# Kernel tuning notes

Hardware: AMD Instinct MI355X
Metric: run time of the kernel (lower is better)

The kernel has to match this reference:

```python
import jax, jax.numpy as jnp
import numpy as np
import math

NUM_HEADS = 16
ATTN_WIDTH = 256


def setup_inputs() -> dict:
    key = jax.random.key(0)
    ks = jax.random.split(key, 5)
    B, S, C, H = 2, 2048, 1024, 1024
    scale = 0.02
    return {
        "x": jax.random.normal(ks[0], (B, S, C), dtype=jnp.float32),
        "Wq": jax.random.normal(ks[1], (C, H), dtype=jnp.float32) * scale,
        "Wk": jax.random.normal(ks[2], (C, H), dtype=jnp.float32) * scale,
        "Wv": jax.random.normal(ks[3], (C, H), dtype=jnp.float32) * scale,
        "Wo": jax.random.normal(ks[4], (H, C), dtype=jnp.float32) * scale,
    }


def reference(x, Wq, Wk, Wv, Wo):
    B, S, C = x.shape
    H = NUM_HEADS
    dh = Wq.shape[1] // H  # head dim; Q.size(-1) in torch code

    def split_heads(t):
        # [B, S, H*dh] -> [B, H, S, dh]
        return t.reshape(B, S, H, dh).transpose(0, 2, 1, 3)

    q = split_heads(x @ Wq)
    k = split_heads(x @ Wk)
    v = split_heads(x @ Wv)

    scores = jnp.einsum("bhqd,bhkd->bhqk", q, k) / math.sqrt(dh)
    # exp-shift (first 'softmax-like' step, unnormalized)
    scores = jnp.exp(scores - jnp.max(scores, axis=-1, keepdims=True))
    # banded mask: tril(attn_width//2 - 1).triu(-(attn_width//2))
    i = jnp.arange(S)[:, None]
    j = jnp.arange(S)[None, :]
    d = j - i
    half = ATTN_WIDTH // 2
    mask = (d <= half - 1) & (d >= -half)
    scores = jnp.where(mask, scores, 0.0)
    # second softmax over the masked exp-scores (zeros contribute exp(0)=1)
    weights = jax.nn.softmax(scores, axis=-1)

    out = jnp.einsum("bhqk,bhkd->bhqd", weights, v)  # [B, H, S, dh]
    out = out.transpose(0, 2, 1, 3).reshape(B, S, H * dh)
    return out @ Wo
```

## Files before the change

kernel.cpp:

```cpp
#include <hip/hip_runtime.h>
#include <math.h>

typedef __bf16 bf16_t;
typedef bf16_t bf16x8 __attribute__((ext_vector_type(8)));
typedef bf16_t bf16x4 __attribute__((ext_vector_type(4)));
typedef float f32x4 __attribute__((ext_vector_type(4)));

constexpr int S_ = 2048;
constexpr float SCALE = 0.125f;

#define MFMA_B16(a, b, c) __builtin_amdgcn_mfma_f32_16x16x32_bf16(a, b, c, 0, 0, 0)

typedef __attribute__((address_space(1))) const void* as1_cvp;
typedef __attribute__((address_space(3))) void* as3_vp;

__device__ __forceinline__ void gl2lds16(const void* g, void* l)
{
    __builtin_amdgcn_global_load_lds((as1_cvp)g, (as3_vp)l, 16, 0, 0);
}

__global__ __launch_bounds__(256) void prep(const float* __restrict__ x,
                                            const float* __restrict__ Wq,
                                            const float* __restrict__ Wk,
                                            const float* __restrict__ Wv,
                                            const float* __restrict__ Wo,
                                            bf16_t* __restrict__ xb,
                                            bf16_t* __restrict__ Wqt,
                                            bf16_t* __restrict__ Wkt,
                                            bf16_t* __restrict__ Wvt,
                                            bf16_t* __restrict__ Wot,
                                            float* __restrict__ vsp)
{
    __shared__ float T[64][65];
    const int blk = blockIdx.x;
    const int tid = threadIdx.x;
    if (blk < 1024) {
#pragma unroll
        for (int u = 0; u < 4; ++u) {
            const int g = blk * 1024 + u * 256 + tid;
            const float4 v = ((const float4*)x)[g];
            bf16x4 o;
            o[0] = (bf16_t)v.x; o[1] = (bf16_t)v.y;
            o[2] = (bf16_t)v.z; o[3] = (bf16_t)v.w;
            *(bf16x4*)&xb[(size_t)g * 4] = o;
        }
    } else if (blk < 2048) {
        const int rem = blk - 1024;
        const int wsel = rem >> 8, t = rem & 255;
        const float* src = (wsel == 0) ? Wq : (wsel == 1) ? Wk : (wsel == 2) ? Wv : Wo;
        bf16_t* dst = (wsel == 0) ? Wqt : (wsel == 1) ? Wkt : (wsel == 2) ? Wvt : Wot;
        const int k0 = (t >> 4) * 64, n0 = (t & 15) * 64;
        const int rr = tid >> 4, c4 = (tid & 15) * 4;
#pragma unroll
        for (int u = 0; u < 4; ++u) {
            const float4 v = *(const float4*)&src[(size_t)(k0 + u * 16 + rr) * 1024 + n0 + c4];
            T[u * 16 + rr][c4 + 0] = v.x; T[u * 16 + rr][c4 + 1] = v.y;
            T[u * 16 + rr][c4 + 2] = v.z; T[u * 16 + rr][c4 + 3] = v.w;
        }
        __syncthreads();
#pragma unroll
        for (int u = 0; u < 4; ++u) {
            bf16x4 o;
#pragma unroll
            for (int e = 0; e < 4; ++e) o[e] = (bf16_t)T[c4 + e][u * 16 + rr];
            *(bf16x4*)&dst[(size_t)(n0 + u * 16 + rr) * 1024 + k0 + c4] = o;
        }
    } else {
#pragma unroll
        for (int u = 0; u < 8; ++u) vsp[u * 256 + tid] = 0.f;
    }
}

template <int MODE>
__device__ __forceinline__ void mfma_gemm_body(const bf16_t* __restrict__ A,
                                               const bf16_t* __restrict__ Bt,
                                               void* __restrict__ dst,
                                               float* __restrict__ vsum_out,
                                               int m0, int n0)
{
    __shared__ bf16_t As[4096];
    __shared__ bf16_t Bs[4096];

    const int tid = threadIdx.x;
    const int lane = tid & 63, wid = tid >> 6;
    const int l15 = lane & 15, quad = lane >> 4;
    const int wm = (wid & 1) * 64, wn = (wid >> 1) * 64;

    const int srow = wid * 32 + (lane >> 2);
    const int scg8 = (lane & 3) * 8;
    const bf16_t* Ag0 = A  + (size_t)(m0 + srow) * 1024 + scg8;
    const bf16_t* Ag1 = A  + (size_t)(m0 + srow + 16) * 1024 + scg8;
    const bf16_t* Bg0 = Bt + (size_t)(n0 + srow) * 1024 + scg8;
    const bf16_t* Bg1 = Bt + (size_t)(n0 + srow + 16) * 1024 + scg8;
    bf16_t* Al0 = As + (wid * 2 + 0) * 512;
    bf16_t* Al1 = As + (wid * 2 + 1) * 512;
    bf16_t* Bl0 = Bs + (wid * 2 + 0) * 512;
    bf16_t* Bl1 = Bs + (wid * 2 + 1) * 512;

    f32x4 acc[4][4];
#pragma unroll
    for (int i = 0; i < 4; ++i)
#pragma unroll
        for (int j = 0; j < 4; ++j) acc[i][j] = (f32x4){0.f, 0.f, 0.f, 0.f};

    for (int k0 = 0; k0 < 1024; k0 += 32) {
        __syncthreads();
        gl2lds16(Ag0 + k0, Al0);
        gl2lds16(Ag1 + k0, Al1);
        gl2lds16(Bg0 + k0, Bl0);
        gl2lds16(Bg1 + k0, Bl1);
        __syncthreads();

        bf16x8 af[4], bfr[4];
#pragma unroll
        for (int mt = 0; mt < 4; ++mt)
            af[mt] = *(const bf16x8*)&As[(wm + mt * 16 + l15) * 32 + quad * 8];
#pragma unroll
        for (int nt = 0; nt < 4; ++nt)
            bfr[nt] = *(const bf16x8*)&Bs[(wn + nt * 16 + l15) * 32 + quad * 8];
#pragma unroll
        for (int mt = 0; mt < 4; ++mt)
#pragma unroll
            for (int nt = 0; nt < 4; ++nt)
                acc[mt][nt] = MFMA_B16(bfr[nt], af[mt], acc[mt][nt]);
    }

#pragma unroll
    for (int mt = 0; mt < 4; ++mt) {
        const int m = m0 + wm + mt * 16 + l15;
#pragma unroll
        for (int nt = 0; nt < 4; ++nt) {
            const int nb = n0 + wn + nt * 16 + quad * 4;
            if (MODE == 0) {
                *(f32x4*)&((float*)dst)[(size_t)m * 1024 + nb] = acc[mt][nt];
            } else {
                const int bb = m >> 11, s = m & 2047;
                const int hh = nb >> 6, d = nb & 63;
                bf16x4 o;
#pragma unroll
                for (int u = 0; u < 4; ++u) o[u] = (bf16_t)acc[mt][nt][u];
                *(bf16x4*)&((bf16_t*)dst)[((size_t)(bb * 16 + hh) * 2048 + s) * 64 + d] = o;
            }
        }
    }

    if (MODE == 1 && vsum_out != nullptr) {
        const int bb = m0 >> 11;
#pragma unroll
        for (int nt = 0; nt < 4; ++nt) {
            f32x4 p = acc[0][nt];
#pragma unroll
            for (int mt = 1; mt < 4; ++mt) {
                p[0] += acc[mt][nt][0]; p[1] += acc[mt][nt][1];
                p[2] += acc[mt][nt][2]; p[3] += acc[mt][nt][3];
            }
#pragma unroll
            for (int st = 1; st < 16; st <<= 1) {
                p[0] += __shfl_xor(p[0], st);
                p[1] += __shfl_xor(p[1], st);
                p[2] += __shfl_xor(p[2], st);
                p[3] += __shfl_xor(p[3], st);
            }
            if (l15 == 0) {
                const int nI = n0 + wn + nt * 16 + quad * 4;
                float* vp = &vsum_out[(bb * 16 + (nI >> 6)) * 64 + (nI & 63)];
                atomicAdd(vp + 0, p[0]);
                atomicAdd(vp + 1, p[1]);
                atomicAdd(vp + 2, p[2]);
                atomicAdd(vp + 3, p[3]);
            }
        }
    }
}

__global__ __launch_bounds__(256) void gemm_qkv_mfma(const bf16_t* __restrict__ xb,
                                                     const bf16_t* __restrict__ Wqt,
                                                     const bf16_t* __restrict__ Wkt,
                                                     const bf16_t* __restrict__ Wvt,
                                                     bf16_t* Qh, bf16_t* Kh, bf16_t* Vh,
                                                     float* vsp)
{
    const bf16_t* Bt = (blockIdx.z == 0) ? Wqt : (blockIdx.z == 1) ? Wkt : Wvt;
    bf16_t* dst = (blockIdx.z == 0) ? Qh : (blockIdx.z == 1) ? Kh : Vh;
    float* vs = (blockIdx.z == 2) ? vsp : nullptr;
    mfma_gemm_body<1>(xb, Bt, dst, vs, blockIdx.y * 128, blockIdx.x * 128);
}

__global__ __launch_bounds__(256) void gemm_out_mfma(const bf16_t* __restrict__ attn,
                                                     const bf16_t* __restrict__ Wot,
                                                     float* __restrict__ out)
{
    mfma_gemm_body<0>(attn, Wot, out, nullptr, blockIdx.y * 128, blockIdx.x * 128);
}

__global__ __launch_bounds__(256) void attn_fused(const bf16_t* __restrict__ Qh,
                                                  const bf16_t* __restrict__ Kh,
                                                  const bf16_t* __restrict__ Vh,
                                                  const float* __restrict__ vsp,
                                                  bf16_t* __restrict__ attn)
{
    __shared__ bf16_t Qs[4096];
    __shared__ bf16_t Kbig[16384];
    __shared__ float msh[4][4][16];
    __shared__ float zsh[4][16];

    bf16_t* Ks2 = Kbig;
    bf16_t* Vt  = Kbig + 4096;
    bf16_t* Wsm = Kbig + 8704;

    const int tid = threadIdx.x;
    const int lane = tid & 63, wid = tid >> 6;
    const int l15 = lane & 15, quad = lane >> 4;
    const int b = blockIdx.z, h = blockIdx.y, bh = b * 16 + h;
    const int i0 = blockIdx.x * 64;
    const bf16_t* Qb = Qh + (size_t)bh * 131072;
    const bf16_t* Kb = Kh + (size_t)bh * 131072;
    const bf16_t* Vb = Vh + (size_t)bh * 131072;

#pragma unroll
    for (int c = 0; c < 2; ++c) {
        const int g = (wid * 2 + c) * 64 + lane;
        const int half = g >> 8, rem = g & 255;
        const int row = rem >> 2, c8 = rem & 3;
        gl2lds16(Qb + (size_t)(i0 + row) * 64 + half * 32 + c8 * 8,
                 Qs + (wid * 2 + c) * 512);
    }
    __syncthreads();

    bf16x8 af[4][2];
#pragma unroll
    for (int mt = 0; mt < 4; ++mt)
#pragma unroll
        for (int ks = 0; ks < 2; ++ks)
            af[mt][ks] = *(const bf16x8*)&Qs[ks * 2048 + (mt * 16 + l15) * 32 + quad * 8];

    float rmax[4] = {-3.0e38f, -3.0e38f, -3.0e38f, -3.0e38f};

    for (int jc = 0; jc < 8; ++jc) {
        __syncthreads();
#pragma unroll
        for (int c = 0; c < 8; ++c) {
            const int g = (wid * 8 + c) * 64 + lane;
            const int half = g >> 10, rem = g & 1023;
            const int row = rem >> 2, c8 = rem & 3;
            gl2lds16(Kb + (size_t)(jc * 256 + row) * 64 + half * 32 + c8 * 8,
                     Kbig + (size_t)(wid * 8 + c) * 512);
        }
        __syncthreads();
#pragma unroll
        for (int ntl = 0; ntl < 4; ++ntl) {
            const int nt = wid * 4 + ntl;
            const bf16x8 b0 = *(const bf16x8*)&Kbig[(nt * 16 + l15) * 32 + quad * 8];
            const bf16x8 b1 = *(const bf16x8*)&Kbig[8192 + (nt * 16 + l15) * 32 + quad * 8];
#pragma unroll
            for (int mt = 0; mt < 4; ++mt) {
                f32x4 t = (f32x4){0.f, 0.f, 0.f, 0.f};
                t = MFMA_B16(b0, af[mt][0], t);
                t = MFMA_B16(b1, af[mt][1], t);
                rmax[mt] = fmaxf(rmax[mt], fmaxf(fmaxf(t[0], t[1]), fmaxf(t[2], t[3])));
            }
        }
    }
#pragma unroll
    for (int mt = 0; mt < 4; ++mt) {
        float v = rmax[mt];
        v = fmaxf(v, __shfl_xor(v, 16));
        v = fmaxf(v, __shfl_xor(v, 32));
        if (quad == 0) msh[wid][mt][l15] = v;
    }
    __syncthreads();

    float mreg[4];
#pragma unroll
    for (int r = 0; r < 4; ++r) {
        const int il = quad * 4 + r;
        mreg[r] = SCALE * fmaxf(fmaxf(msh[0][wid][il], msh[1][wid][il]),
                                fmaxf(msh[2][wid][il], msh[3][wid][il]));
    }

    const bf16x8 aq0 = *(const bf16x8*)&Qs[(wid * 16 + l15) * 32 + quad * 8];
    const bf16x8 aq1 = *(const bf16x8*)&Qs[2048 + (wid * 16 + l15) * 32 + quad * 8];

    f32x4 vsd4[4];
#pragma unroll
    for (int nt = 0; nt < 4; ++nt)
        vsd4[nt] = *(const f32x4*)&vsp[bh * 64 + nt * 16 + quad * 4];

    f32x4 accO[4];
#pragma unroll
    for (int nt = 0; nt < 4; ++nt) accO[nt] = (f32x4){0.f, 0.f, 0.f, 0.f};
    float zp[4] = {0.f, 0.f, 0.f, 0.f};

    for (int cb = 0; cb < 5; ++cb) {
        const int jb = i0 - 128 + cb * 64;
        if (jb < 0 || jb >= S_) continue;

        __syncthreads();
#pragma unroll
        for (int c = 0; c < 2; ++c) {
            const int g = (wid * 2 + c) * 64 + lane;
            const int half = g >> 8, rem = g & 255;
            const int row = rem >> 2, c8 = rem & 3;
            gl2lds16(Kb + (size_t)(jb + row) * 64 + half * 32 + c8 * 8,
                     Ks2 + (wid * 2 + c) * 512);
        }
        {
            const bf16x8 v0 = *(const bf16x8*)&Vb[(size_t)(jb + lane) * 64 + wid * 16];
            const bf16x8 v1 = *(const bf16x8*)&Vb[(size_t)(jb + lane) * 64 + wid * 16 + 8];
#pragma unroll
            for (int e = 0; e < 8; ++e) {
                Vt[(wid * 16 + e) * 72 + lane] = v0[e];
                Vt[(wid * 16 + 8 + e) * 72 + lane] = v1[e];
            }
        }
        __syncthreads();

        f32x4 sacc[4];
#pragma unroll
        for (int nt = 0; nt < 4; ++nt) {
            const bf16x8 k0 = *(const bf16x8*)&Ks2[(nt * 16 + l15) * 32 + quad * 8];
            const bf16x8 k1 = *(const bf16x8*)&Ks2[2048 + (nt * 16 + l15) * 32 + quad * 8];
            f32x4 t = (f32x4){0.f, 0.f, 0.f, 0.f};
            t = MFMA_B16(aq0, k0, t);
            t = MFMA_B16(aq1, k1, t);
            sacc[nt] = t;
        }

#pragma unroll
        for (int nt = 0; nt < 4; ++nt) {
#pragma unroll
            for (int r = 0; r < 4; ++r) {
                const int ig = i0 + wid * 16 + quad * 4 + r;
                const int jg = jb + nt * 16 + l15;
                const int dd = jg - ig;
                const bool ok = (dd >= -128) && (dd <= 127);
                const float t = __expf(sacc[nt][r] * SCALE - mreg[r]);
                const float wv = ok ? (__expf(t) - 1.0f) : 0.0f;
                const bf16_t wb = (bf16_t)wv;
                zp[r] += (float)wb;
                Wsm[(wid * 16 + quad * 4 + r) * 72 + nt * 16 + l15] = wb;
            }
        }
        __syncthreads();

#pragma unroll
        for (int ks = 0; ks < 2; ++ks) {
            const bf16x8 aw = *(const bf16x8*)&Wsm[(wid * 16 + l15) * 72 + ks * 32 + quad * 8];
#pragma unroll
            for (int nt = 0; nt < 4; ++nt) {
                const bf16x8 bv = *(const bf16x8*)&Vt[(nt * 16 + l15) * 72 + ks * 32 + quad * 8];
                accO[nt] = MFMA_B16(bv, aw, accO[nt]);
            }
        }
    }

#pragma unroll
    for (int r = 0; r < 4; ++r) {
        float z = zp[r];
        z += __shfl_xor(z, 1);
        z += __shfl_xor(z, 2);
        z += __shfl_xor(z, 4);
        z += __shfl_xor(z, 8);
        if (l15 == 0) zsh[wid][quad * 4 + r] = z + (float)S_;
    }
    __syncthreads();
    const float rz = 1.0f / zsh[wid][l15];

    const int irow = i0 + wid * 16 + l15;
#pragma unroll
    for (int nt = 0; nt < 4; ++nt) {
        bf16x4 o;
#pragma unroll
        for (int r = 0; r < 4; ++r)
            o[r] = (bf16_t)((accO[nt][r] + vsd4[nt][r]) * rz);
        *(bf16x4*)&attn[(size_t)(b * S_ + irow) * 1024 + h * 64 + nt * 16 + quad * 4] = o;
    }
}

extern "C" void kernel_launch(void* const* d_in, const int* in_sizes, int n_in,
                              void* d_out, int out_size, void* d_ws, size_t ws_size,
                              hipStream_t stream)
{
    const float* x  = (const float*)d_in[0];
    const float* Wq = (const float*)d_in[1];
    const float* Wk = (const float*)d_in[2];
    const float* Wv = (const float*)d_in[3];
    const float* Wo = (const float*)d_in[4];
    float* out = (float*)d_out;

    char* ws = (char*)d_ws;
    bf16_t* xb   = (bf16_t*)(ws + 0);
    bf16_t* Wqt  = (bf16_t*)(ws + 8388608);
    bf16_t* Wkt  = (bf16_t*)(ws + 10485760);
    bf16_t* Wvt  = (bf16_t*)(ws + 12582912);
    bf16_t* Wot  = (bf16_t*)(ws + 14680064);
    bf16_t* Qh   = (bf16_t*)(ws + 16777216);
    bf16_t* Kh   = (bf16_t*)(ws + 25165824);
    bf16_t* Vh   = (bf16_t*)(ws + 33554432);
    bf16_t* attn = (bf16_t*)(ws + 41943040);
    float*  vsp  = (float*)(ws + 50331648);

    prep<<<2049, 256, 0, stream>>>(x, Wq, Wk, Wv, Wo, xb, Wqt, Wkt, Wvt, Wot, vsp);
    gemm_qkv_mfma<<<dim3(8, 32, 3), 256, 0, stream>>>(xb, Wqt, Wkt, Wvt, Qh, Kh, Vh, vsp);
    attn_fused<<<dim3(32, 16, 2), 256, 0, stream>>>(Qh, Kh, Vh, vsp, attn);
    gemm_out_mfma<<<dim3(8, 32), 256, 0, stream>>>(attn, Wot, out);
}
```

Before: 193.3 us.

## Double attention query tile to 128 rows and remap blocks for locality

Each attention block now handles 128 query rows instead of 64, with each wave owning two 16-row tiles. This halves the number of blocks that stream the full K sequence for the row-max pass, and lets each loaded V tile be reused across two query tiles. The grid is flattened to 512 blocks with an index remap that places consecutive blocks on different heads of the same batch, likely aimed at L2 locality. The cost is higher register pressure (Q fragments for 8 tiles, doubled accumulators) and fewer blocks to fill the GPU, partly offset by launch_bounds(256,2).

```diff
diff --git a/kernel.cpp b/kernel.cpp
--- a/kernel.cpp
+++ b/kernel.cpp
@@ -193,67 +193,73 @@
     mfma_gemm_body<0>(attn, Wot, out, nullptr, blockIdx.y * 128, blockIdx.x * 128);
 }
 
-__global__ __launch_bounds__(256) void attn_fused(const bf16_t* __restrict__ Qh,
-                                                  const bf16_t* __restrict__ Kh,
-                                                  const bf16_t* __restrict__ Vh,
-                                                  const float* __restrict__ vsp,
-                                                  bf16_t* __restrict__ attn)
-{
-    __shared__ bf16_t Qs[4096];
-    __shared__ bf16_t Kbig[16384];
-    __shared__ float msh[4][4][16];
-    __shared__ float zsh[4][16];
-
-    bf16_t* Ks2 = Kbig;
-    bf16_t* Vt  = Kbig + 4096;
-    bf16_t* Wsm = Kbig + 8704;
+__global__ __launch_bounds__(256, 2) void attn_fused(const bf16_t* __restrict__ Qh,
+                                                     const bf16_t* __restrict__ Kh,
+                                                     const bf16_t* __restrict__ Vh,
+                                                     const float* __restrict__ vsp,
+                                                     bf16_t* __restrict__ attn)
+{
+    __shared__ bf16_t Qs[8192];
+    __shared__ bf16_t pool[17920];
+    __shared__ float msh[4][8][16];
+    __shared__ float zsh[4][32];
+
+    bf16_t* Ks2 = pool;
+    bf16_t* Vt  = pool + 4096;
+    bf16_t* Ws  = pool + 8704;
 
     const int tid = threadIdx.x;
     const int lane = tid & 63, wid = tid >> 6;
     const int l15 = lane & 15, quad = lane >> 4;
-    const int b = blockIdx.z, h = blockIdx.y, bh = b * 16 + h;
-    const int i0 = blockIdx.x * 64;
+
+    const int f = blockIdx.x;
+    const int seq = f >> 3;
+    const int bh = (f & 7) + 8 * (seq >> 4);
+    const int i0 = (seq & 15) * 128;
+    const int b = bh >> 4, h = bh & 15;
     const bf16_t* Qb = Qh + (size_t)bh * 131072;
     const bf16_t* Kb = Kh + (size_t)bh * 131072;
     const bf16_t* Vb = Vh + (size_t)bh * 131072;
 
 #pragma unroll
-    for (int c = 0; c < 2; ++c) {
-        const int g = (wid * 2 + c) * 64 + lane;
-        const int half = g >> 8, rem = g & 255;
-        const int row = rem >> 2, c8 = rem & 3;
-        gl2lds16(Qb + (size_t)(i0 + row) * 64 + half * 32 + c8 * 8,
-                 Qs + (wid * 2 + c) * 512);
+    for (int c = 0; c < 4; ++c) {
+        const int g = wid * 4 + c;
+        const int half = g >> 3;
+        const int row = (g & 7) * 16 + (lane >> 2);
+        gl2lds16(Qb + (size_t)(i0 + row) * 64 + half * 32 + (lane & 3) * 8,
+                 Qs + g * 512);
     }
     __syncthreads();
 
-    bf16x8 af[4][2];
-#pragma unroll
-    for (int mt = 0; mt < 4; ++mt)
+    bf16x8 af[8][2];
+#pragma unroll
+    for (int mt = 0; mt < 8; ++mt)
 #pragma unroll
         for (int ks = 0; ks < 2; ++ks)
-            af[mt][ks] = *(const bf16x8*)&Qs[ks * 2048 + (mt * 16 + l15) * 32 + quad * 8];
-
-    float rmax[4] = {-3.0e38f, -3.0e38f, -3.0e38f, -3.0e38f};
+            af[mt][ks] = *(const bf16x8*)&Qs[ks * 4096 + (mt * 16 + l15) * 32 + quad * 8];
+
+    float rmax[8];
+#pragma unroll
+    for (int mt = 0; mt < 8; ++mt) rmax[mt] = -3.0e38f;
 
     for (int jc = 0; jc < 8; ++jc) {
         __syncthreads();
 #pragma unroll
         for (int c = 0; c < 8; ++c) {
-            const int g = (wid * 8 + c) * 64 + lane;
-            const int half = g >> 10, rem = g & 1023;
-            const int row = rem >> 2, c8 = rem & 3;
-            gl2lds16(Kb + (size_t)(jc * 256 + row) * 64 + half * 32 + c8 * 8,
-                     Kbig + (size_t)(wid * 8 + c) * 512);
+            const int g = wid * 8 + c;
+            const int half = g >> 4;
+            const int row = (g & 15) * 16 + (lane >> 2);
+            gl2lds16(Kb + (size_t)(jc * 256 + row) * 64 + half * 32 + (lane & 3) * 8,
+                     pool + g * 512);
         }
         __syncthreads();
 #pragma unroll
         for (int ntl = 0; ntl < 4; ++ntl) {
-            const int nt = wid * 4 + ntl;
-            const bf16x8 b0 = *(const bf16x8*)&Kbig[(nt * 16 + l15) * 32 + quad * 8];
-            const bf16x8 b1 = *(const bf16x8*)&Kbig[8192 + (nt * 16 + l15) * 32 + quad * 8];
-#pragma unroll
-            for (int mt = 0; mt < 4; ++mt) {
+            const int jt = wid * 4 + ntl;
+            const bf16x8 b0 = *(const bf16x8*)&pool[(jt * 16 + l15) * 32 + quad * 8];
+            const bf16x8 b1 = *(const bf16x8*)&pool[8192 + (jt * 16 + l15) * 32 + quad * 8];
+#pragma unroll
+            for (int mt = 0; mt < 8; ++mt) {
                 f32x4 t = (f32x4){0.f, 0.f, 0.f, 0.f};
                 t = MFMA_B16(b0, af[mt][0], t);
                 t = MFMA_B16(b1, af[mt][1], t);
@@ -262,7 +268,7 @@
         }
     }
 #pragma unroll
-    for (int mt = 0; mt < 4; ++mt) {
+    for (int mt = 0; mt < 8; ++mt) {
         float v = rmax[mt];
         v = fmaxf(v, __shfl_xor(v, 16));
         v = fmaxf(v, __shfl_xor(v, 32));
@@ -270,39 +276,41 @@
     }
     __syncthreads();
 
-    float mreg[4];
-#pragma unroll
-    for (int r = 0; r < 4; ++r) {
-        const int il = quad * 4 + r;
-        mreg[r] = SCALE * fmaxf(fmaxf(msh[0][wid][il], msh[1][wid][il]),
-                                fmaxf(msh[2][wid][il], msh[3][wid][il]));
-    }
-
-    const bf16x8 aq0 = *(const bf16x8*)&Qs[(wid * 16 + l15) * 32 + quad * 8];
-    const bf16x8 aq1 = *(const bf16x8*)&Qs[2048 + (wid * 16 + l15) * 32 + quad * 8];
+    float mreg[2][4];
+#pragma unroll
+    for (int t = 0; t < 2; ++t)
+#pragma unroll
+        for (int r = 0; r < 4; ++r) {
+            const int mt = wid * 2 + t;
+            const int il = quad * 4 + r;
+            mreg[t][r] = SCALE * fmaxf(fmaxf(msh[0][mt][il], msh[1][mt][il]),
+                                       fmaxf(msh[2][mt][il], msh[3][mt][il]));
+        }
 
     f32x4 vsd4[4];
 #pragma unroll
-    for (int nt = 0; nt < 4; ++nt)
-        vsd4[nt] = *(const f32x4*)&vsp[bh * 64 + nt * 16 + quad * 4];
-
-    f32x4 accO[4];
-#pragma unroll
-    for (int nt = 0; nt < 4; ++nt) accO[nt] = (f32x4){0.f, 0.f, 0.f, 0.f};
-    float zp[4] = {0.f, 0.f, 0.f, 0.f};
-
-    for (int cb = 0; cb < 5; ++cb) {
+    for (int dt = 0; dt < 4; ++dt)
+        vsd4[dt] = *(const f32x4*)&vsp[bh * 64 + dt * 16 + quad * 4];
+
+    f32x4 accO[2][4];
+#pragma unroll
+    for (int t = 0; t < 2; ++t)
+#pragma unroll
+        for (int dt = 0; dt < 4; ++dt) accO[t][dt] = (f32x4){0.f, 0.f, 0.f, 0.f};
+    float zp[2][4] = {{0.f, 0.f, 0.f, 0.f}, {0.f, 0.f, 0.f, 0.f}};
+
+    for (int cb = 0; cb < 6; ++cb) {
         const int jb = i0 - 128 + cb * 64;
         if (jb < 0 || jb >= S_) continue;
 
         __syncthreads();
 #pragma unroll
         for (int c = 0; c < 2; ++c) {
-            const int g = (wid * 2 + c) * 64 + lane;
-            const int half = g >> 8, rem = g & 255;
-            const int row = rem >> 2, c8 = rem & 3;
-            gl2lds16(Kb + (size_t)(jb + row) * 64 + half * 32 + c8 * 8,
-                     Ks2 + (wid * 2 + c) * 512);
+            const int g = wid * 2 + c;
+            const int half = g >> 2;
+            const int row = (g & 3) * 16 + (lane >> 2);
+            gl2lds16(Kb + (size_t)(jb + row) * 64 + half * 32 + (lane & 3) * 8,
+                     Ks2 + g * 512);
         }
         {
             const bf16x8 v0 = *(const bf16x8*)&Vb[(size_t)(jb + lane) * 64 + wid * 16];
@@ -315,65 +323,74 @@
         }
         __syncthreads();
 
-        f32x4 sacc[4];
-#pragma unroll
-        for (int nt = 0; nt < 4; ++nt) {
-            const bf16x8 k0 = *(const bf16x8*)&Ks2[(nt * 16 + l15) * 32 + quad * 8];
-            const bf16x8 k1 = *(const bf16x8*)&Ks2[2048 + (nt * 16 + l15) * 32 + quad * 8];
-            f32x4 t = (f32x4){0.f, 0.f, 0.f, 0.f};
-            t = MFMA_B16(aq0, k0, t);
-            t = MFMA_B16(aq1, k1, t);
-            sacc[nt] = t;
-        }
-
-#pragma unroll
-        for (int nt = 0; nt < 4; ++nt) {
-#pragma unroll
-            for (int r = 0; r < 4; ++r) {
-                const int ig = i0 + wid * 16 + quad * 4 + r;
-                const int jg = jb + nt * 16 + l15;
-                const int dd = jg - ig;
-                const bool ok = (dd >= -128) && (dd <= 127);
-                const float t = __expf(sacc[nt][r] * SCALE - mreg[r]);
-                const float wv = ok ? (__expf(t) - 1.0f) : 0.0f;
-                const bf16_t wb = (bf16_t)wv;
-                zp[r] += (float)wb;
-                Wsm[(wid * 16 + quad * 4 + r) * 72 + nt * 16 + l15] = wb;
+#pragma unroll
+        for (int t = 0; t < 2; ++t) {
+            const int mt = wid * 2 + t;
+#pragma unroll
+            for (int jt4 = 0; jt4 < 4; ++jt4) {
+                const bf16x8 k0 = *(const bf16x8*)&Ks2[(jt4 * 16 + l15) * 32 + quad * 8];
+                const bf16x8 k1 = *(const bf16x8*)&Ks2[2048 + (jt4 * 16 + l15) * 32 + quad * 8];
+                f32x4 sc = (f32x4){0.f, 0.f, 0.f, 0.f};
+                sc = MFMA_B16(af[mt][0], k0, sc);
+                sc = MFMA_B16(af[mt][1], k1, sc);
+#pragma unroll
+                for (int r = 0; r < 4; ++r) {
+                    const int ig = i0 + mt * 16 + quad * 4 + r;
+                    const int jg = jb + jt4 * 16 + l15;
+                    const int dd = jg - ig;
+                    const bool ok = (dd >= -128) && (dd <= 127);
+                    const float e1 = __expf(sc[r] * SCALE - mreg[t][r]);
+                    const float wv = ok ? (__expf(e1) - 1.0f) : 0.0f;
+                    const bf16_t wb = (bf16_t)wv;
+                    zp[t][r] += (float)wb;
+                    Ws[(mt * 16 + quad * 4 + r) * 72 + jt4 * 16 + l15] = wb;
+                }
             }
         }
         __syncthreads();
 
 #pragma unroll
         for (int ks = 0; ks < 2; ++ks) {
-            const bf16x8 aw = *(const bf16x8*)&Wsm[(wid * 16 + l15) * 72 + ks * 32 + quad * 8];
-#pragma unroll
-            for (int nt = 0; nt < 4; ++nt) {
-                const bf16x8 bv = *(const bf16x8*)&Vt[(nt * 16 + l15) * 72 + ks * 32 + quad * 8];
-                accO[nt] = MFMA_B16(bv, aw, accO[nt]);
-            }
-        }
-    }
-
-#pragma unroll
-    for (int r = 0; r < 4; ++r) {
-        float z = zp[r];
-        z += __shfl_xor(z, 1);
-        z += __shfl_xor(z, 2);
-        z += __shfl_xor(z, 4);
-        z += __shfl_xor(z, 8);
-        if (l15 == 0) zsh[wid][quad * 4 + r] = z + (float)S_;
-    }
+            bf16x8 bv[4];
+#pragma unroll
+            for (int dt = 0; dt < 4; ++dt)
+                bv[dt] = *(const bf16x8*)&Vt[(dt * 16 + l15) * 72 + ks * 32 + quad * 8];
+#pragma unroll
+            for (int t = 0; t < 2; ++t) {
+                const int mt = wid * 2 + t;
+                const bf16x8 aw = *(const bf16x8*)&Ws[(mt * 16 + l15) * 72 + ks * 32 + quad * 8];
+#pragma unroll
+                for (int dt = 0; dt < 4; ++dt)
+                    accO[t][dt] = MFMA_B16(bv[dt], aw, accO[t][dt]);
+            }
+        }
+    }
+
+#pragma unroll
+    for (int t = 0; t < 2; ++t)
+#pragma unroll
+        for (int r = 0; r < 4; ++r) {
+            float z = zp[t][r];
+            z += __shfl_xor(z, 1);
+            z += __shfl_xor(z, 2);
+            z += __shfl_xor(z, 4);
+            z += __shfl_xor(z, 8);
+            if (l15 == 0) zsh[wid][t * 16 + quad * 4 + r] = z + (float)S_;
+        }
     __syncthreads();
-    const float rz = 1.0f / zsh[wid][l15];
-
-    const int irow = i0 + wid * 16 + l15;
-#pragma unroll
-    for (int nt = 0; nt < 4; ++nt) {
-        bf16x4 o;
-#pragma unroll
-        for (int r = 0; r < 4; ++r)
-            o[r] = (bf16_t)((accO[nt][r] + vsd4[nt][r]) * rz);
-        *(bf16x4*)&attn[(size_t)(b * S_ + irow) * 1024 + h * 64 + nt * 16 + quad * 4] = o;
+
+#pragma unroll
+    for (int t = 0; t < 2; ++t) {
+        const float rz = 1.0f / zsh[wid][t * 16 + l15];
+        const int irow = i0 + (wid * 2 + t) * 16 + l15;
+#pragma unroll
+        for (int dt = 0; dt < 4; ++dt) {
+            bf16x4 o;
+#pragma unroll
+            for (int r = 0; r < 4; ++r)
+                o[r] = (bf16_t)((accO[t][dt][r] + vsd4[dt][r]) * rz);
+            *(bf16x4*)&attn[(size_t)(b * S_ + irow) * 1024 + h * 64 + dt * 16 + quad * 4] = o;
+        }
     }
 }
 
@@ -402,6 +419,6 @@
 
     prep<<<2049, 256, 0, stream>>>(x, Wq, Wk, Wv, Wo, xb, Wqt, Wkt, Wvt, Wot, vsp);
     gemm_qkv_mfma<<<dim3(8, 32, 3), 256, 0, stream>>>(xb, Wqt, Wkt, Wvt, Qh, Kh, Vh, vsp);
-    attn_fused<<<dim3(32, 16, 2), 256, 0, stream>>>(Qh, Kh, Vh, vsp, attn);
+    attn_fused<<<512, 256, 0, stream>>>(Qh, Kh, Vh, vsp, attn);
     gemm_out_mfma<<<dim3(8, 32), 256, 0, stream>>>(attn, Wot, out);
 }
```

Measured after the change: 189.2 us. 2.1% less time.
